# Kernel optimization log

Measured on AMD Instinct MI355X. Metric: run time of the kernel, lower is better.

## Reference

```python
import jax, jax.numpy as jnp
import numpy as np

D_MODEL = 1024
N_HEAD = 16


def setup_inputs() -> dict:
    key = jax.random.key(0)
    ks = jax.random.split(key, 9)
    d = D_MODEL
    s = 0.02
    return {
        "x": jax.random.normal(ks[0], (4, 2048, d), dtype=jnp.float32),
        "w_q": jax.random.normal(ks[1], (d, d), dtype=jnp.float32) * s,
        "b_q": jax.random.normal(ks[2], (d,), dtype=jnp.float32) * s,
        "w_k": jax.random.normal(ks[3], (d, d), dtype=jnp.float32) * s,
        "b_k": jax.random.normal(ks[4], (d,), dtype=jnp.float32) * s,
        "w_v": jax.random.normal(ks[5], (d, d), dtype=jnp.float32) * s,
        "b_v": jax.random.normal(ks[6], (d,), dtype=jnp.float32) * s,
        "w_o": jax.random.normal(ks[7], (d, d), dtype=jnp.float32) * s,
        "b_o": jax.random.normal(ks[8], (d,), dtype=jnp.float32) * s,
    }


def reference(x, w_q, b_q, w_k, b_k, w_v, b_v, w_o, b_o):
    B, S, D = x.shape
    H = N_HEAD
    dh = D // H

    def split(t):  # [B,S,D] -> [B,H,S,dh]
        return t.reshape(B, S, H, dh).transpose(0, 2, 1, 3)

    q = split(x @ w_q + b_q)
    k = split(x @ w_k + b_k)
    v = split(x @ w_v + b_v)

    scale = 1.0 / jnp.sqrt(jnp.float32(dh))
    score = jnp.einsum("bhqd,bhkd->bhqk", q, k) * scale
    score = jax.nn.softmax(score, axis=-1)
    out = jnp.einsum("bhqk,bhkd->bhqd", score, v)
    out = out.transpose(0, 2, 1, 3).reshape(B, S, D)
    return out @ w_o + b_o
```

## Files before the change

kernel.cpp:

```cpp
#include <hip/hip_runtime.h>


typedef __bf16 bf16x8 __attribute__((ext_vector_type(8)));
typedef float f32x4 __attribute__((ext_vector_type(4)));
typedef float f32x16 __attribute__((ext_vector_type(16)));
typedef unsigned short u16x8 __attribute__((ext_vector_type(8)));
typedef unsigned u32x4 __attribute__((ext_vector_type(4)));
typedef unsigned u32x2 __attribute__((ext_vector_type(2)));

#define SEQ 2048
#define DM 1024
#define NHEAD 16
#define MTOT 8192
#define QSCALE 0.18033688011112042f

__device__ __forceinline__ unsigned short f2bf(float f) {
  unsigned u = __builtin_bit_cast(unsigned, f);
  u += 0x7fffu + ((u >> 16) & 1u);
  return (unsigned short)(u >> 16);
}

__device__ __forceinline__ unsigned pkbf(float lo, float hi) {
  __bf16 a = (__bf16)lo, b = (__bf16)hi;
  return ((unsigned)__builtin_bit_cast(unsigned short, b) << 16) |
         __builtin_bit_cast(unsigned short, a);
}

__device__ __forceinline__ void async16(const void* g, void* l) {
  __builtin_amdgcn_global_load_lds(
      (const __attribute__((address_space(1))) void*)g,
      (__attribute__((address_space(3))) void*)l, 16, 0, 0);
}

template <bool CX>
__device__ __forceinline__ void exch(unsigned A, unsigned B, unsigned& fr0, unsigned& fr2) {
#if __has_builtin(__builtin_amdgcn_permlane32_swap)
  if constexpr (CX) {
    u32x2 r = __builtin_amdgcn_permlane32_swap(B, A, false, false);
    fr0 = r[1]; fr2 = r[0];
  } else {
    u32x2 r = __builtin_amdgcn_permlane32_swap(A, B, false, false);
    fr0 = r[0]; fr2 = r[1];
  }
#else
  int hi = (threadIdx.x & 63) >> 5;
  unsigned sA = (unsigned)__shfl_xor((int)A, 32);
  unsigned sB = (unsigned)__shfl_xor((int)B, 32);
  fr0 = hi ? sB : A;
  fr2 = hi ? B : sA;
#endif
}

__device__ __forceinline__ float halfsum(float rs) {
#if __has_builtin(__builtin_amdgcn_permlane32_swap)
  unsigned rb = __builtin_bit_cast(unsigned, rs);
  u32x2 rr = __builtin_amdgcn_permlane32_swap(rb, rb, false, false);
  return __builtin_bit_cast(float, rr[0]) + __builtin_bit_cast(float, rr[1]);
#else
  return rs + __shfl_xor(rs, 32);
#endif
}

__global__ __launch_bounds__(256) void k_cvt(const float* __restrict__ x,
                                             unsigned short* __restrict__ xb) {
  size_t i = ((size_t)blockIdx.x * 256 + threadIdx.x) * 8;
  float4 a = *(const float4*)(x + i);
  float4 b = *(const float4*)(x + i + 4);
  u16x8 o;
  o[0] = f2bf(a.x); o[1] = f2bf(a.y); o[2] = f2bf(a.z); o[3] = f2bf(a.w);
  o[4] = f2bf(b.x); o[5] = f2bf(b.y); o[6] = f2bf(b.z); o[7] = f2bf(b.w);
  *(u16x8*)(xb + i) = o;
}

__global__ __launch_bounds__(256) void k_wt(const float* __restrict__ w0, const float* __restrict__ w1,
                                            const float* __restrict__ w2, const float* __restrict__ w3,
                                            unsigned short* __restrict__ t0, unsigned short* __restrict__ t1,
                                            unsigned short* __restrict__ t2, unsigned short* __restrict__ t3) {
  __shared__ float t[64][65];
  int z = blockIdx.z;
  const float* w = z == 0 ? w0 : z == 1 ? w1 : z == 2 ? w2 : w3;
  unsigned short* wt = z == 0 ? t0 : z == 1 ? t1 : z == 2 ? t2 : t3;
  int nt = blockIdx.x, kt = blockIdx.y;
  int tx = threadIdx.x & 63, ty = threadIdx.x >> 6;
  for (int i = 0; i < 16; ++i) {
    int r = i * 4 + ty;
    t[r][tx] = w[(size_t)(kt * 64 + r) * DM + nt * 64 + tx];
  }
  __syncthreads();
  for (int i = 0; i < 16; ++i) {
    int r = i * 4 + ty;
    wt[(size_t)(nt * 64 + r) * DM + kt * 64 + tx] = f2bf(t[tx][r]);
  }
}

__device__ __forceinline__ void gemm_body(const unsigned short* __restrict__ A,
                                          const unsigned short* __restrict__ Bt,
                                          const float* __restrict__ bias,
                                          unsigned short* __restrict__ Cb,
                                          float* __restrict__ Cf, int bm, int bn, float sc) {
  __shared__ __align__(16) unsigned short As[128 * 64];
  __shared__ __align__(16) unsigned short Bs[128 * 64];
  const int K = DM, N = DM;
  int tid = threadIdx.x, w = tid >> 6, l = tid & 63;
  int g = l >> 4, l15 = l & 15;
  int wm = (w >> 1) * 64, wn = (w & 1) * 64;
  f32x4 acc[4][4];
#pragma unroll
  for (int mi = 0; mi < 4; ++mi)
#pragma unroll
    for (int ni = 0; ni < 4; ++ni)
#pragma unroll
      for (int e = 0; e < 4; ++e) acc[mi][ni][e] = 0.f;

  int lr8 = l >> 3, lp = l & 7;
  for (int kt = 0; kt < K / 64; ++kt) {
    __syncthreads();
#pragma unroll
    for (int i = 0; i < 4; ++i) {
      int cs = i * 4 + w;
      int row = cs * 8 + lr8;
      int c = lp ^ lr8;
      async16(A + (size_t)(bm + row) * K + kt * 64 + c * 8, &As[cs * 512]);
      async16(Bt + (size_t)(bn + row) * K + kt * 64 + c * 8, &Bs[cs * 512]);
    }
    __syncthreads();
    bf16x8 af[4][2];
#pragma unroll
    for (int mi = 0; mi < 4; ++mi)
#pragma unroll
      for (int kk = 0; kk < 2; ++kk) {
        int row = wm + mi * 16 + l15;
        af[mi][kk] = *(const bf16x8*)&As[row * 64 + (((kk * 4 + g) ^ (row & 7)) * 8)];
      }
    __builtin_amdgcn_s_setprio(1);
#pragma unroll
    for (int ni = 0; ni < 4; ++ni) {
      int row = wn + ni * 16 + l15;
      bf16x8 b0 = *(const bf16x8*)&Bs[row * 64 + (((0 + g) ^ (row & 7)) * 8)];
      bf16x8 b1 = *(const bf16x8*)&Bs[row * 64 + (((4 + g) ^ (row & 7)) * 8)];
#pragma unroll
      for (int mi = 0; mi < 4; ++mi) {
        acc[mi][ni] = __builtin_amdgcn_mfma_f32_16x16x32_bf16(af[mi][0], b0, acc[mi][ni], 0, 0, 0);
        acc[mi][ni] = __builtin_amdgcn_mfma_f32_16x16x32_bf16(af[mi][1], b1, acc[mi][ni], 0, 0, 0);
      }
    }
    __builtin_amdgcn_s_setprio(0);
  }
  float bv[4];
#pragma unroll
  for (int ni = 0; ni < 4; ++ni) bv[ni] = bias[bn + wn + ni * 16 + l15];
#pragma unroll
  for (int mi = 0; mi < 4; ++mi)
#pragma unroll
    for (int ni = 0; ni < 4; ++ni) {
      int col = bn + wn + ni * 16 + l15;
#pragma unroll
      for (int r = 0; r < 4; ++r) {
        int rowg = bm + wm + mi * 16 + g * 4 + r;
        float v = (acc[mi][ni][r] + bv[ni]) * sc;
        if (Cf) Cf[(size_t)rowg * N + col] = v;
        else    Cb[(size_t)rowg * N + col] = f2bf(v);
      }
    }
}

__global__ __launch_bounds__(256) void k_gemm(const unsigned short* __restrict__ A,
                                              const unsigned short* __restrict__ Bt,
                                              const float* __restrict__ bias,
                                              unsigned short* __restrict__ Cb,
                                              float* __restrict__ Cf) {
  gemm_body(A, Bt, bias, Cb, Cf, blockIdx.y * 128, blockIdx.x * 128, 1.f);
}

__global__ __launch_bounds__(256) void k_gemm_qkv(const unsigned short* __restrict__ A,
                                                  const unsigned short* bt0, const unsigned short* bt1,
                                                  const unsigned short* bt2,
                                                  const float* b0, const float* b1, const float* b2,
                                                  unsigned short* o0, unsigned short* o1,
                                                  unsigned short* o2) {
  int which = blockIdx.x >> 3;
  const unsigned short* Bt = which == 0 ? bt0 : which == 1 ? bt1 : bt2;
  const float* bias = which == 0 ? b0 : which == 1 ? b1 : b2;
  unsigned short* Cb = which == 0 ? o0 : which == 1 ? o1 : o2;
  float sc = which == 0 ? QSCALE : 1.f;
  gemm_body(A, Bt, bias, Cb, nullptr, blockIdx.y * 128, (blockIdx.x & 7) * 128, sc);
}

__global__ __launch_bounds__(256) void k_vt(const unsigned short* __restrict__ V,
                                            unsigned short* __restrict__ Vt) {
  __shared__ __align__(16) unsigned short t[64 * 64];
  int st = blockIdx.x, bh = blockIdx.y;
  int b = bh >> 4, h = bh & 15;
  int tid = threadIdx.x, w = tid >> 6, l = tid & 63;
  for (int i = 0; i < 2; ++i) {
    int cs = i * 4 + w;
    int row = cs * 8 + (l >> 3);
    int c = l & 7;
    async16(V + ((size_t)(b * SEQ + st * 64 + row) * DM + h * 64 + c * 8), &t[cs * 512]);
  }
  __syncthreads();
  for (int p = 0; p < 2; ++p) {
    int d = p * 32 + (tid >> 3);
    int cs = tid & 7;
    u16x8 o;
    for (int j = 0; j < 8; ++j) o[j] = t[(cs * 8 + j) * 64 + d];
    *(u16x8*)(Vt + ((size_t)bh * 64 + d) * SEQ + st * 64 + cs * 8) = o;
  }
}

template <bool CX>
__device__ __forceinline__ void attn_core(const unsigned short* __restrict__ Q,
                                          const unsigned short* __restrict__ Kg,
                                          const unsigned short* __restrict__ Vt,
                                          unsigned short* __restrict__ Og,
                                          unsigned short* smem, int b, int h, int bh, int qt) {
  int tid = threadIdx.x, w = tid >> 6, l = tid & 63;
  int l31 = l & 31, hi = l >> 5, l7 = l & 7;
  int lr8 = l >> 3, lp = l & 7;
  int q0w = qt * 256 + w * 64;
  unsigned short* const KS = smem;
  unsigned short* const VS = smem + 16384;

  bf16x8 qf[2][4];
#pragma unroll
  for (int qh = 0; qh < 2; ++qh)
#pragma unroll
    for (int c = 0; c < 4; ++c)
      qf[qh][c] = *(const bf16x8*)(Q + (size_t)(b * SEQ + q0w + qh * 32 + l31) * DM +
                                   h * 64 + c * 16 + hi * 8);

  const f32x16 fz = {0.f, 0.f, 0.f, 0.f, 0.f, 0.f, 0.f, 0.f,
                     0.f, 0.f, 0.f, 0.f, 0.f, 0.f, 0.f, 0.f};
  float lrow[2] = {0.f, 0.f};
  f32x16 oacc[2][2];
#pragma unroll
  for (int qh = 0; qh < 2; ++qh)
#pragma unroll
    for (int d = 0; d < 2; ++d) oacc[qh][d] = fz;

  auto stage = [&](int kt) {
    int s = kt & 3;
    unsigned short* kd = KS + s * 4096;
    unsigned short* vd = VS + s * 4096;
#pragma unroll
    for (int i = 0; i < 2; ++i) {
      int cs = i * 4 + w;
      int row = cs * 8 + lr8;
      int c = lp ^ lr8;
      async16(Kg + ((size_t)(b * SEQ + kt * 64 + row) * DM + h * 64 + c * 8), kd + cs * 512);
      async16(Vt + (((size_t)bh * 64 + row) * SEQ + kt * 64 + c * 8), vd + cs * 512);
    }
  };

  auto compute = [&](int kt) {
    const unsigned short* kc = KS + (kt & 3) * 4096;
    const unsigned short* vc = VS + (kt & 3) * 4096;

    f32x16 sacc[2][2];
    __builtin_amdgcn_s_setprio(1);
#pragma unroll
    for (int kh = 0; kh < 2; ++kh) {
      const unsigned short* kb = kc + (kh * 32 + l31) * 64;
      bf16x8 a0 = *(const bf16x8*)(kb + ((hi ^ l7) << 3));
      sacc[0][kh] = __builtin_amdgcn_mfma_f32_32x32x16_bf16(a0, qf[0][0], fz, 0, 0, 0);
      sacc[1][kh] = __builtin_amdgcn_mfma_f32_32x32x16_bf16(a0, qf[1][0], fz, 0, 0, 0);
#pragma unroll
      for (int c = 1; c < 4; ++c) {
        bf16x8 a = *(const bf16x8*)(kb + (((2 * c + hi) ^ l7) << 3));
        sacc[0][kh] = __builtin_amdgcn_mfma_f32_32x32x16_bf16(a, qf[0][c], sacc[0][kh], 0, 0, 0);
        sacc[1][kh] = __builtin_amdgcn_mfma_f32_32x32x16_bf16(a, qf[1][c], sacc[1][kh], 0, 0, 0);
      }
    }
    __builtin_amdgcn_s_setprio(0);

    bf16x8 pf[2][4];
#pragma unroll
    for (int qh = 0; qh < 2; ++qh) {
      float r0 = 0.f, r1 = 0.f, r2 = 0.f, r3 = 0.f;
#pragma unroll
      for (int kh = 0; kh < 2; ++kh)
#pragma unroll
        for (int e = 0; e < 16; e += 4) {
          float p0 = __builtin_amdgcn_exp2f(sacc[qh][kh][e + 0]);
          float p1 = __builtin_amdgcn_exp2f(sacc[qh][kh][e + 1]);
          float p2 = __builtin_amdgcn_exp2f(sacc[qh][kh][e + 2]);
          float p3 = __builtin_amdgcn_exp2f(sacc[qh][kh][e + 3]);
          sacc[qh][kh][e + 0] = p0; sacc[qh][kh][e + 1] = p1;
          sacc[qh][kh][e + 2] = p2; sacc[qh][kh][e + 3] = p3;
          r0 += p0; r1 += p1; r2 += p2; r3 += p3;
        }
      lrow[qh] += halfsum((r0 + r1) + (r2 + r3));
#pragma unroll
      for (int ks = 0; ks < 4; ++ks) {
        int kh = ks >> 1, q4 = (ks & 1) * 8;
        unsigned A0 = pkbf(sacc[qh][kh][q4 + 0], sacc[qh][kh][q4 + 1]);
        unsigned A1 = pkbf(sacc[qh][kh][q4 + 2], sacc[qh][kh][q4 + 3]);
        unsigned B0 = pkbf(sacc[qh][kh][q4 + 4], sacc[qh][kh][q4 + 5]);
        unsigned B1 = pkbf(sacc[qh][kh][q4 + 6], sacc[qh][kh][q4 + 7]);
        unsigned f0, f1, f2, f3;
        exch<CX>(A0, B0, f0, f2);
        exch<CX>(A1, B1, f1, f3);
        u32x4 fr; fr[0] = f0; fr[1] = f1; fr[2] = f2; fr[3] = f3;
        pf[qh][ks] = __builtin_bit_cast(bf16x8, fr);
      }
    }

    __builtin_amdgcn_s_setprio(1);
#pragma unroll
    for (int d = 0; d < 2; ++d) {
      const unsigned short* vb = vc + (d * 32 + l31) * 64;
#pragma unroll
      for (int ks = 0; ks < 4; ++ks) {
        bf16x8 a = *(const bf16x8*)(vb + (((2 * ks + hi) ^ l7) << 3));
        oacc[0][d] = __builtin_amdgcn_mfma_f32_32x32x16_bf16(a, pf[0][ks], oacc[0][d], 0, 0, 0);
        oacc[1][d] = __builtin_amdgcn_mfma_f32_32x32x16_bf16(a, pf[1][ks], oacc[1][d], 0, 0, 0);
      }
    }
    __builtin_amdgcn_s_setprio(0);
  };

#define VWAIT4 asm volatile("s_waitcnt vmcnt(4)" ::: "memory")
#define VWAIT0 asm volatile("s_waitcnt vmcnt(0)" ::: "memory")
#define BARR                         \
  __builtin_amdgcn_s_barrier();      \
  __builtin_amdgcn_sched_barrier(0)

  stage(0);
  stage(1);
  VWAIT4;
  BARR;
  const int NT = SEQ / 64;
  for (int kt = 0; kt < NT - 2; ++kt) {
    stage(kt + 2);
    compute(kt);
    VWAIT4;
    BARR;
  }
  compute(NT - 2);
  VWAIT0;
  BARR;
  compute(NT - 1);
  BARR;

#undef VWAIT4
#undef VWAIT0
#undef BARR

  unsigned* ot = (unsigned*)smem + w * (32 * 33);
#pragma unroll
  for (int qh = 0; qh < 2; ++qh) {
    float inv = 1.f / lrow[qh];
#pragma unroll
    for (int d = 0; d < 2; ++d)
#pragma unroll
      for (int qd = 0; qd < 4; ++qd) {
        unsigned u0 = pkbf(oacc[qh][d][qd * 4 + 0] * inv, oacc[qh][d][qd * 4 + 1] * inv);
        unsigned u1 = pkbf(oacc[qh][d][qd * 4 + 2] * inv, oacc[qh][d][qd * 4 + 3] * inv);
        int idx = l31 * 33 + d * 16 + qd * 4 + hi * 2;
        ot[idx] = u0;
        ot[idx + 1] = u1;
      }
    int row = l >> 1, half = l & 1;
    const unsigned* sr = (const unsigned*)smem + w * (32 * 33) + row * 33 + half * 16;
    unsigned o[16];
#pragma unroll
    for (int j = 0; j < 16; ++j) o[j] = sr[j];
    size_t gbase = (size_t)(b * SEQ + q0w + qh * 32 + row) * DM + h * 64 + half * 32;
#pragma unroll
    for (int i = 0; i < 4; ++i) {
      u32x4 t;
      t[0] = o[i * 4 + 0]; t[1] = o[i * 4 + 1]; t[2] = o[i * 4 + 2]; t[3] = o[i * 4 + 3];
      *(u32x4*)(Og + gbase + i * 8) = t;
    }
  }
}

__global__ __launch_bounds__(256, 2) void k_attn(const unsigned short* __restrict__ Q,
                                                 const unsigned short* __restrict__ Kg,
                                                 const unsigned short* __restrict__ Vt,
                                                 unsigned short* __restrict__ Og) {
  __shared__ __align__(16) unsigned short smem[32768];
  int bh = blockIdx.x, qt = blockIdx.y;
  int b = bh >> 4, h = bh & 15;
#if __has_builtin(__builtin_amdgcn_permlane32_swap)
  unsigned lid = threadIdx.x & 63;
  u32x2 pr = __builtin_amdgcn_permlane32_swap(lid, lid + 64u, false, false);
  bool convX = __builtin_amdgcn_readfirstlane(pr[0]) >= 64u;
#else
  bool convX = false;
#endif
  if (convX) attn_core<true>(Q, Kg, Vt, Og, smem, b, h, bh, qt);
  else       attn_core<false>(Q, Kg, Vt, Og, smem, b, h, bh, qt);
}

extern "C" void kernel_launch(void* const* d_in, const int* in_sizes, int n_in,
                              void* d_out, int out_size, void* d_ws, size_t ws_size,
                              hipStream_t stream) {
  const float* x  = (const float*)d_in[0];
  const float* wq = (const float*)d_in[1];
  const float* bq = (const float*)d_in[2];
  const float* wk = (const float*)d_in[3];
  const float* bk = (const float*)d_in[4];
  const float* wv = (const float*)d_in[5];
  const float* bv = (const float*)d_in[6];
  const float* wo = (const float*)d_in[7];
  const float* bo = (const float*)d_in[8];

  const size_t SZ_X = (size_t)MTOT * DM * 2;
  const size_t SZ_W = (size_t)DM * DM * 2;
  char* ws = (char*)d_ws;
  size_t off = 0;
  unsigned short* xb  = (unsigned short*)(ws + off); off += SZ_X;
  unsigned short* wqT = (unsigned short*)(ws + off); off += SZ_W;
  unsigned short* wkT = (unsigned short*)(ws + off); off += SZ_W;
  unsigned short* wvT = (unsigned short*)(ws + off); off += SZ_W;
  unsigned short* woT = (unsigned short*)(ws + off); off += SZ_W;
  unsigned short* Qb  = (unsigned short*)(ws + off); off += SZ_X;
  unsigned short* Kb  = (unsigned short*)(ws + off); off += SZ_X;
  unsigned short* Vb  = (unsigned short*)(ws + off); off += SZ_X;
  unsigned short* Vtb = (unsigned short*)(ws + off); off += SZ_X;
  unsigned short* Ab  = (unsigned short*)(ws + off); off += SZ_X;
  if (ws_size < off) return;

  k_cvt<<<dim3(4096), dim3(256), 0, stream>>>(x, xb);
  k_wt<<<dim3(16, 16, 4), dim3(256), 0, stream>>>(wq, wk, wv, wo, wqT, wkT, wvT, woT);
  k_gemm_qkv<<<dim3(24, 64), dim3(256), 0, stream>>>(xb, wqT, wkT, wvT, bq, bk, bv, Qb, Kb, Vb);
  k_vt<<<dim3(32, 64), dim3(256), 0, stream>>>(Vb, Vtb);
  k_attn<<<dim3(64, 8), dim3(256), 0, stream>>>(Qb, Kb, Vtb, Ab);
  k_gemm<<<dim3(8, 64), dim3(256), 0, stream>>>(Ab, woT, bo, nullptr, (float*)d_out);
}
```

Measured before the change: 181.9 us.

## Fuse V transpose into QKV GEMM epilogue and software-pipeline PV with QK^T

The V projection blocks of the QKV GEMM now write their output directly in the transposed [b,h,d,s] layout, so the separate k_vt transpose kernel and the intermediate V buffer are removed. In the attention kernel, the per-tile compute is split into QK^T, softmax and PV stages, and the loop is restructured so the PV of tile t-1 is issued alongside the QK^T of tile t. This lets matrix ops overlap the softmax latency. In exchange, the transposed epilogue does strided 8-byte stores, and the pipelined loop keeps extra probability fragments live, adding register pressure.

```diff
diff --git a/kernel.cpp b/kernel.cpp
--- a/kernel.cpp
+++ b/kernel.cpp
@@ -5,6 +5,7 @@
 typedef float f32x4 __attribute__((ext_vector_type(4)));
 typedef float f32x16 __attribute__((ext_vector_type(16)));
 typedef unsigned short u16x8 __attribute__((ext_vector_type(8)));
+typedef unsigned short u16x4 __attribute__((ext_vector_type(4)));
 typedef unsigned u32x4 __attribute__((ext_vector_type(4)));
 typedef unsigned u32x2 __attribute__((ext_vector_type(2)));
 
@@ -97,7 +98,9 @@
                                           const unsigned short* __restrict__ Bt,
                                           const float* __restrict__ bias,
                                           unsigned short* __restrict__ Cb,
-                                          float* __restrict__ Cf, int bm, int bn, float sc) {
+                                          float* __restrict__ Cf,
+                                          unsigned short* __restrict__ Vt,
+                                          int bm, int bn, float sc) {
   __shared__ __align__(16) unsigned short As[128 * 64];
   __shared__ __align__(16) unsigned short Bs[128 * 64];
   const int K = DM, N = DM;
@@ -149,6 +152,22 @@
   float bv[4];
 #pragma unroll
   for (int ni = 0; ni < 4; ++ni) bv[ni] = bias[bn + wn + ni * 16 + l15];
+  if (Vt) {
+#pragma unroll
+    for (int mi = 0; mi < 4; ++mi)
+#pragma unroll
+      for (int ni = 0; ni < 4; ++ni) {
+        int col = bn + wn + ni * 16 + l15;
+        int bh16 = (col >> 6), d = col & 63;
+        int rowg = bm + wm + mi * 16 + g * 4;
+        int b = rowg >> 11, s = rowg & 2047;
+        u16x4 pk;
+#pragma unroll
+        for (int r = 0; r < 4; ++r) pk[r] = f2bf((acc[mi][ni][r] + bv[ni]) * sc);
+        *(u16x4*)(Vt + ((size_t)((b * NHEAD + bh16) * 64 + d)) * SEQ + s) = pk;
+      }
+    return;
+  }
 #pragma unroll
   for (int mi = 0; mi < 4; ++mi)
 #pragma unroll
@@ -169,7 +188,7 @@
                                               const float* __restrict__ bias,
                                               unsigned short* __restrict__ Cb,
                                               float* __restrict__ Cf) {
-  gemm_body(A, Bt, bias, Cb, Cf, blockIdx.y * 128, blockIdx.x * 128, 1.f);
+  gemm_body(A, Bt, bias, Cb, Cf, nullptr, blockIdx.y * 128, blockIdx.x * 128, 1.f);
 }
 
 __global__ __launch_bounds__(256) void k_gemm_qkv(const unsigned short* __restrict__ A,
@@ -177,35 +196,14 @@
                                                   const unsigned short* bt2,
                                                   const float* b0, const float* b1, const float* b2,
                                                   unsigned short* o0, unsigned short* o1,
-                                                  unsigned short* o2) {
+                                                  unsigned short* vt) {
   int which = blockIdx.x >> 3;
   const unsigned short* Bt = which == 0 ? bt0 : which == 1 ? bt1 : bt2;
   const float* bias = which == 0 ? b0 : which == 1 ? b1 : b2;
-  unsigned short* Cb = which == 0 ? o0 : which == 1 ? o1 : o2;
+  unsigned short* Cb = which == 0 ? o0 : which == 1 ? o1 : nullptr;
+  unsigned short* Vt = which == 2 ? vt : nullptr;
   float sc = which == 0 ? QSCALE : 1.f;
-  gemm_body(A, Bt, bias, Cb, nullptr, blockIdx.y * 128, (blockIdx.x & 7) * 128, sc);
-}
-
-__global__ __launch_bounds__(256) void k_vt(const unsigned short* __restrict__ V,
-                                            unsigned short* __restrict__ Vt) {
-  __shared__ __align__(16) unsigned short t[64 * 64];
-  int st = blockIdx.x, bh = blockIdx.y;
-  int b = bh >> 4, h = bh & 15;
-  int tid = threadIdx.x, w = tid >> 6, l = tid & 63;
-  for (int i = 0; i < 2; ++i) {
-    int cs = i * 4 + w;
-    int row = cs * 8 + (l >> 3);
-    int c = l & 7;
-    async16(V + ((size_t)(b * SEQ + st * 64 + row) * DM + h * 64 + c * 8), &t[cs * 512]);
-  }
-  __syncthreads();
-  for (int p = 0; p < 2; ++p) {
-    int d = p * 32 + (tid >> 3);
-    int cs = tid & 7;
-    u16x8 o;
-    for (int j = 0; j < 8; ++j) o[j] = t[(cs * 8 + j) * 64 + d];
-    *(u16x8*)(Vt + ((size_t)bh * 64 + d) * SEQ + st * 64 + cs * 8) = o;
-  }
+  gemm_body(A, Bt, bias, Cb, nullptr, Vt, blockIdx.y * 128, (blockIdx.x & 7) * 128, sc);
 }
 
 template <bool CX>
@@ -237,6 +235,7 @@
   for (int qh = 0; qh < 2; ++qh)
 #pragma unroll
     for (int d = 0; d < 2; ++d) oacc[qh][d] = fz;
+  bf16x8 pf[2][4];
 
   auto stage = [&](int kt) {
     int s = kt & 3;
@@ -252,12 +251,8 @@
     }
   };
 
-  auto compute = [&](int kt) {
+  auto qkt = [&](int kt, f32x16 (&sacc)[2][2]) {
     const unsigned short* kc = KS + (kt & 3) * 4096;
-    const unsigned short* vc = VS + (kt & 3) * 4096;
-
-    f32x16 sacc[2][2];
-    __builtin_amdgcn_s_setprio(1);
 #pragma unroll
     for (int kh = 0; kh < 2; ++kh) {
       const unsigned short* kb = kc + (kh * 32 + l31) * 64;
@@ -271,9 +266,23 @@
         sacc[1][kh] = __builtin_amdgcn_mfma_f32_32x32x16_bf16(a, qf[1][c], sacc[1][kh], 0, 0, 0);
       }
     }
-    __builtin_amdgcn_s_setprio(0);
-
-    bf16x8 pf[2][4];
+  };
+
+  auto pv = [&](int kt) {
+    const unsigned short* vc = VS + (kt & 3) * 4096;
+#pragma unroll
+    for (int d = 0; d < 2; ++d) {
+      const unsigned short* vb = vc + (d * 32 + l31) * 64;
+#pragma unroll
+      for (int ks = 0; ks < 4; ++ks) {
+        bf16x8 a = *(const bf16x8*)(vb + (((2 * ks + hi) ^ l7) << 3));
+        oacc[0][d] = __builtin_amdgcn_mfma_f32_32x32x16_bf16(a, pf[0][ks], oacc[0][d], 0, 0, 0);
+        oacc[1][d] = __builtin_amdgcn_mfma_f32_32x32x16_bf16(a, pf[1][ks], oacc[1][d], 0, 0, 0);
+      }
+    }
+  };
+
+  auto softmax = [&](f32x16 (&sacc)[2][2]) {
 #pragma unroll
     for (int qh = 0; qh < 2; ++qh) {
       float r0 = 0.f, r1 = 0.f, r2 = 0.f, r3 = 0.f;
@@ -304,19 +313,6 @@
         pf[qh][ks] = __builtin_bit_cast(bf16x8, fr);
       }
     }
-
-    __builtin_amdgcn_s_setprio(1);
-#pragma unroll
-    for (int d = 0; d < 2; ++d) {
-      const unsigned short* vb = vc + (d * 32 + l31) * 64;
-#pragma unroll
-      for (int ks = 0; ks < 4; ++ks) {
-        bf16x8 a = *(const bf16x8*)(vb + (((2 * ks + hi) ^ l7) << 3));
-        oacc[0][d] = __builtin_amdgcn_mfma_f32_32x32x16_bf16(a, pf[0][ks], oacc[0][d], 0, 0, 0);
-        oacc[1][d] = __builtin_amdgcn_mfma_f32_32x32x16_bf16(a, pf[1][ks], oacc[1][d], 0, 0, 0);
-      }
-    }
-    __builtin_amdgcn_s_setprio(0);
   };
 
 #define VWAIT4 asm volatile("s_waitcnt vmcnt(4)" ::: "memory")
@@ -325,21 +321,35 @@
   __builtin_amdgcn_s_barrier();      \
   __builtin_amdgcn_sched_barrier(0)
 
+  const int NT = SEQ / 64;
   stage(0);
   stage(1);
   VWAIT4;
   BARR;
-  const int NT = SEQ / 64;
-  for (int kt = 0; kt < NT - 2; ++kt) {
-    stage(kt + 2);
-    compute(kt);
+  {
+    f32x16 sacc[2][2];
+    stage(2);
+    __builtin_amdgcn_s_setprio(1);
+    qkt(0, sacc);
+    __builtin_amdgcn_s_setprio(0);
+    softmax(sacc);
     VWAIT4;
     BARR;
   }
-  compute(NT - 2);
-  VWAIT0;
-  BARR;
-  compute(NT - 1);
+  for (int t = 1; t < NT; ++t) {
+    f32x16 sacc[2][2];
+    if (t + 2 < NT) stage(t + 2);
+    __builtin_amdgcn_s_setprio(1);
+    pv(t - 1);
+    qkt(t, sacc);
+    __builtin_amdgcn_s_setprio(0);
+    softmax(sacc);
+    if (t + 2 < NT) { VWAIT4; } else { VWAIT0; }
+    BARR;
+  }
+  __builtin_amdgcn_s_setprio(1);
+  pv(NT - 1);
+  __builtin_amdgcn_s_setprio(0);
   BARR;
 
 #undef VWAIT4
@@ -417,15 +427,13 @@
   unsigned short* woT = (unsigned short*)(ws + off); off += SZ_W;
   unsigned short* Qb  = (unsigned short*)(ws + off); off += SZ_X;
   unsigned short* Kb  = (unsigned short*)(ws + off); off += SZ_X;
-  unsigned short* Vb  = (unsigned short*)(ws + off); off += SZ_X;
   unsigned short* Vtb = (unsigned short*)(ws + off); off += SZ_X;
   unsigned short* Ab  = (unsigned short*)(ws + off); off += SZ_X;
   if (ws_size < off) return;
 
   k_cvt<<<dim3(4096), dim3(256), 0, stream>>>(x, xb);
   k_wt<<<dim3(16, 16, 4), dim3(256), 0, stream>>>(wq, wk, wv, wo, wqT, wkT, wvT, woT);
-  k_gemm_qkv<<<dim3(24, 64), dim3(256), 0, stream>>>(xb, wqT, wkT, wvT, bq, bk, bv, Qb, Kb, Vb);
-  k_vt<<<dim3(32, 64), dim3(256), 0, stream>>>(Vb, Vtb);
+  k_gemm_qkv<<<dim3(24, 64), dim3(256), 0, stream>>>(xb, wqT, wkT, wvT, bq, bk, bv, Qb, Kb, Vtb);
   k_attn<<<dim3(64, 8), dim3(256), 0, stream>>>(Qb, Kb, Vtb, Ab);
   k_gemm<<<dim3(8, 64), dim3(256), 0, stream>>>(Ab, woT, bo, nullptr, (float*)d_out);
 }
```

New measurement: 183.5 us. About the same (+0.9%).

## Halve attention query tile per wave and simplify K/V pipeline to double buffering

Applied to the files above, without the earlier changes.

Each wave now handles 32 query rows instead of 64, so the attention grid doubles to 1024 blocks, LDS drops to 32KB, and launch bounds ask for 4 blocks per CU. The 4-stage async K/V ring with hand-tuned vmcnt waits is replaced by a 2-stage buffer synchronised with __syncthreads each tile. The aim is more occupancy and fewer registers per wave. In exchange, every K/V tile loaded into LDS now serves half as many queries, doubling K/V traffic, and the full barrier each iteration may expose load latency.

```diff
diff --git a/kernel.cpp b/kernel.cpp
--- a/kernel.cpp
+++ b/kernel.cpp
@@ -217,29 +217,23 @@
   int tid = threadIdx.x, w = tid >> 6, l = tid & 63;
   int l31 = l & 31, hi = l >> 5, l7 = l & 7;
   int lr8 = l >> 3, lp = l & 7;
-  int q0w = qt * 256 + w * 64;
+  int q0w = qt * 128 + w * 32;
   unsigned short* const KS = smem;
-  unsigned short* const VS = smem + 16384;
-
-  bf16x8 qf[2][4];
-#pragma unroll
-  for (int qh = 0; qh < 2; ++qh)
-#pragma unroll
-    for (int c = 0; c < 4; ++c)
-      qf[qh][c] = *(const bf16x8*)(Q + (size_t)(b * SEQ + q0w + qh * 32 + l31) * DM +
-                                   h * 64 + c * 16 + hi * 8);
+  unsigned short* const VS = smem + 8192;
+
+  bf16x8 qf[4];
+#pragma unroll
+  for (int c = 0; c < 4; ++c)
+    qf[c] = *(const bf16x8*)(Q + (size_t)(b * SEQ + q0w + l31) * DM + h * 64 + c * 16 + hi * 8);
 
   const f32x16 fz = {0.f, 0.f, 0.f, 0.f, 0.f, 0.f, 0.f, 0.f,
                      0.f, 0.f, 0.f, 0.f, 0.f, 0.f, 0.f, 0.f};
-  float lrow[2] = {0.f, 0.f};
-  f32x16 oacc[2][2];
-#pragma unroll
-  for (int qh = 0; qh < 2; ++qh)
-#pragma unroll
-    for (int d = 0; d < 2; ++d) oacc[qh][d] = fz;
+  float lrow = 0.f;
+  f32x16 oacc[2];
+  oacc[0] = fz; oacc[1] = fz;
 
   auto stage = [&](int kt) {
-    int s = kt & 3;
+    int s = kt & 1;
     unsigned short* kd = KS + s * 4096;
     unsigned short* vd = VS + s * 4096;
 #pragma unroll
@@ -252,56 +246,58 @@
     }
   };
 
-  auto compute = [&](int kt) {
-    const unsigned short* kc = KS + (kt & 3) * 4096;
-    const unsigned short* vc = VS + (kt & 3) * 4096;
-
-    f32x16 sacc[2][2];
+  const int NT = SEQ / 64;
+  stage(0);
+  __syncthreads();
+  for (int t = 0; t < NT; ++t) {
+    int cur = t & 1;
+    if (t + 1 < NT) stage(t + 1);
+    const unsigned short* kc = KS + cur * 4096;
+    const unsigned short* vc = VS + cur * 4096;
+
+    f32x16 sacc[2];
     __builtin_amdgcn_s_setprio(1);
 #pragma unroll
     for (int kh = 0; kh < 2; ++kh) {
       const unsigned short* kb = kc + (kh * 32 + l31) * 64;
       bf16x8 a0 = *(const bf16x8*)(kb + ((hi ^ l7) << 3));
-      sacc[0][kh] = __builtin_amdgcn_mfma_f32_32x32x16_bf16(a0, qf[0][0], fz, 0, 0, 0);
-      sacc[1][kh] = __builtin_amdgcn_mfma_f32_32x32x16_bf16(a0, qf[1][0], fz, 0, 0, 0);
+      sacc[kh] = __builtin_amdgcn_mfma_f32_32x32x16_bf16(a0, qf[0], fz, 0, 0, 0);
 #pragma unroll
       for (int c = 1; c < 4; ++c) {
         bf16x8 a = *(const bf16x8*)(kb + (((2 * c + hi) ^ l7) << 3));
-        sacc[0][kh] = __builtin_amdgcn_mfma_f32_32x32x16_bf16(a, qf[0][c], sacc[0][kh], 0, 0, 0);
-        sacc[1][kh] = __builtin_amdgcn_mfma_f32_32x32x16_bf16(a, qf[1][c], sacc[1][kh], 0, 0, 0);
+        sacc[kh] = __builtin_amdgcn_mfma_f32_32x32x16_bf16(a, qf[c], sacc[kh], 0, 0, 0);
       }
     }
     __builtin_amdgcn_s_setprio(0);
 
-    bf16x8 pf[2][4];
-#pragma unroll
-    for (int qh = 0; qh < 2; ++qh) {
+    bf16x8 pf[4];
+    {
       float r0 = 0.f, r1 = 0.f, r2 = 0.f, r3 = 0.f;
 #pragma unroll
       for (int kh = 0; kh < 2; ++kh)
 #pragma unroll
         for (int e = 0; e < 16; e += 4) {
-          float p0 = __builtin_amdgcn_exp2f(sacc[qh][kh][e + 0]);
-          float p1 = __builtin_amdgcn_exp2f(sacc[qh][kh][e + 1]);
-          float p2 = __builtin_amdgcn_exp2f(sacc[qh][kh][e + 2]);
-          float p3 = __builtin_amdgcn_exp2f(sacc[qh][kh][e + 3]);
-          sacc[qh][kh][e + 0] = p0; sacc[qh][kh][e + 1] = p1;
-          sacc[qh][kh][e + 2] = p2; sacc[qh][kh][e + 3] = p3;
+          float p0 = __builtin_amdgcn_exp2f(sacc[kh][e + 0]);
+          float p1 = __builtin_amdgcn_exp2f(sacc[kh][e + 1]);
+          float p2 = __builtin_amdgcn_exp2f(sacc[kh][e + 2]);
+          float p3 = __builtin_amdgcn_exp2f(sacc[kh][e + 3]);
+          sacc[kh][e + 0] = p0; sacc[kh][e + 1] = p1;
+          sacc[kh][e + 2] = p2; sacc[kh][e + 3] = p3;
           r0 += p0; r1 += p1; r2 += p2; r3 += p3;
         }
-      lrow[qh] += halfsum((r0 + r1) + (r2 + r3));
+      lrow += halfsum((r0 + r1) + (r2 + r3));
 #pragma unroll
       for (int ks = 0; ks < 4; ++ks) {
         int kh = ks >> 1, q4 = (ks & 1) * 8;
-        unsigned A0 = pkbf(sacc[qh][kh][q4 + 0], sacc[qh][kh][q4 + 1]);
-        unsigned A1 = pkbf(sacc[qh][kh][q4 + 2], sacc[qh][kh][q4 + 3]);
-        unsigned B0 = pkbf(sacc[qh][kh][q4 + 4], sacc[qh][kh][q4 + 5]);
-        unsigned B1 = pkbf(sacc[qh][kh][q4 + 6], sacc[qh][kh][q4 + 7]);
+        unsigned A0 = pkbf(sacc[kh][q4 + 0], sacc[kh][q4 + 1]);
+        unsigned A1 = pkbf(sacc[kh][q4 + 2], sacc[kh][q4 + 3]);
+        unsigned B0 = pkbf(sacc[kh][q4 + 4], sacc[kh][q4 + 5]);
+        unsigned B1 = pkbf(sacc[kh][q4 + 6], sacc[kh][q4 + 7]);
         unsigned f0, f1, f2, f3;
         exch<CX>(A0, B0, f0, f2);
         exch<CX>(A1, B1, f1, f3);
         u32x4 fr; fr[0] = f0; fr[1] = f1; fr[2] = f2; fr[3] = f3;
-        pf[qh][ks] = __builtin_bit_cast(bf16x8, fr);
+        pf[ks] = __builtin_bit_cast(bf16x8, fr);
       }
     }
 
@@ -312,60 +308,32 @@
 #pragma unroll
       for (int ks = 0; ks < 4; ++ks) {
         bf16x8 a = *(const bf16x8*)(vb + (((2 * ks + hi) ^ l7) << 3));
-        oacc[0][d] = __builtin_amdgcn_mfma_f32_32x32x16_bf16(a, pf[0][ks], oacc[0][d], 0, 0, 0);
-        oacc[1][d] = __builtin_amdgcn_mfma_f32_32x32x16_bf16(a, pf[1][ks], oacc[1][d], 0, 0, 0);
+        oacc[d] = __builtin_amdgcn_mfma_f32_32x32x16_bf16(a, pf[ks], oacc[d], 0, 0, 0);
       }
     }
     __builtin_amdgcn_s_setprio(0);
-  };
-
-#define VWAIT4 asm volatile("s_waitcnt vmcnt(4)" ::: "memory")
-#define VWAIT0 asm volatile("s_waitcnt vmcnt(0)" ::: "memory")
-#define BARR                         \
-  __builtin_amdgcn_s_barrier();      \
-  __builtin_amdgcn_sched_barrier(0)
-
-  stage(0);
-  stage(1);
-  VWAIT4;
-  BARR;
-  const int NT = SEQ / 64;
-  for (int kt = 0; kt < NT - 2; ++kt) {
-    stage(kt + 2);
-    compute(kt);
-    VWAIT4;
-    BARR;
-  }
-  compute(NT - 2);
-  VWAIT0;
-  BARR;
-  compute(NT - 1);
-  BARR;
-
-#undef VWAIT4
-#undef VWAIT0
-#undef BARR
-
+    __syncthreads();
+  }
+
+  float inv = 1.f / lrow;
   unsigned* ot = (unsigned*)smem + w * (32 * 33);
 #pragma unroll
-  for (int qh = 0; qh < 2; ++qh) {
-    float inv = 1.f / lrow[qh];
-#pragma unroll
-    for (int d = 0; d < 2; ++d)
-#pragma unroll
-      for (int qd = 0; qd < 4; ++qd) {
-        unsigned u0 = pkbf(oacc[qh][d][qd * 4 + 0] * inv, oacc[qh][d][qd * 4 + 1] * inv);
-        unsigned u1 = pkbf(oacc[qh][d][qd * 4 + 2] * inv, oacc[qh][d][qd * 4 + 3] * inv);
-        int idx = l31 * 33 + d * 16 + qd * 4 + hi * 2;
-        ot[idx] = u0;
-        ot[idx + 1] = u1;
-      }
+  for (int d = 0; d < 2; ++d)
+#pragma unroll
+    for (int qd = 0; qd < 4; ++qd) {
+      unsigned u0 = pkbf(oacc[d][qd * 4 + 0] * inv, oacc[d][qd * 4 + 1] * inv);
+      unsigned u1 = pkbf(oacc[d][qd * 4 + 2] * inv, oacc[d][qd * 4 + 3] * inv);
+      int idx = l31 * 33 + d * 16 + qd * 4 + hi * 2;
+      ot[idx] = u0;
+      ot[idx + 1] = u1;
+    }
+  {
     int row = l >> 1, half = l & 1;
     const unsigned* sr = (const unsigned*)smem + w * (32 * 33) + row * 33 + half * 16;
     unsigned o[16];
 #pragma unroll
     for (int j = 0; j < 16; ++j) o[j] = sr[j];
-    size_t gbase = (size_t)(b * SEQ + q0w + qh * 32 + row) * DM + h * 64 + half * 32;
+    size_t gbase = (size_t)(b * SEQ + q0w + row) * DM + h * 64 + half * 32;
 #pragma unroll
     for (int i = 0; i < 4; ++i) {
       u32x4 t;
@@ -375,11 +343,11 @@
   }
 }
 
-__global__ __launch_bounds__(256, 2) void k_attn(const unsigned short* __restrict__ Q,
+__global__ __launch_bounds__(256, 4) void k_attn(const unsigned short* __restrict__ Q,
                                                  const unsigned short* __restrict__ Kg,
                                                  const unsigned short* __restrict__ Vt,
                                                  unsigned short* __restrict__ Og) {
-  __shared__ __align__(16) unsigned short smem[32768];
+  __shared__ __align__(16) unsigned short smem[16384];
   int bh = blockIdx.x, qt = blockIdx.y;
   int b = bh >> 4, h = bh & 15;
 #if __has_builtin(__builtin_amdgcn_permlane32_swap)
@@ -426,6 +394,6 @@
   k_wt<<<dim3(16, 16, 4), dim3(256), 0, stream>>>(wq, wk, wv, wo, wqT, wkT, wvT, woT);
   k_gemm_qkv<<<dim3(24, 64), dim3(256), 0, stream>>>(xb, wqT, wkT, wvT, bq, bk, bv, Qb, Kb, Vb);
   k_vt<<<dim3(32, 64), dim3(256), 0, stream>>>(Vb, Vtb);
-  k_attn<<<dim3(64, 8), dim3(256), 0, stream>>>(Qb, Kb, Vtb, Ab);
+  k_attn<<<dim3(64, 16), dim3(256), 0, stream>>>(Qb, Kb, Vtb, Ab);
   k_gemm<<<dim3(8, 64), dim3(256), 0, stream>>>(Ab, woT, bo, nullptr, (float*)d_out);
 }
```

Result: no change. 185.2 us (+1.9%).
